# Performance work log

Hardware: AMD Instinct MI355X
Metric: run time of the kernel (lower is better)

The kernel has to match this reference:

```python
import jax, jax.numpy as jnp
import numpy as np

B, T, C = 2, 2048, 1024
N_HEAD = 16
G_NON = 32   # qgroup_size_non (layernorm / residual path)
G_LIN = 32   # qgroup_size_lin (linear path)
QMAX = 127.0
EPS = 1e-5


def quantize(x, G):
    """Group-wise symmetric int8 quantization along the last dim.
    Returns q (int8, same shape as x) and scales s with shape x.shape[:-1] + (D//G,)."""
    shp = x.shape
    xg = x.reshape(shp[:-1] + (shp[-1] // G, G))
    s = jnp.maximum(jnp.max(jnp.abs(xg), axis=-1) / QMAX, 1e-8)
    q = jnp.clip(jnp.round(xg / s[..., None]), -QMAX, QMAX).astype(jnp.int8)
    return q.reshape(shp), s


def dequant(q, s, G):
    shp = q.shape
    xg = q.astype(jnp.float32).reshape(shp[:-1] + (shp[-1] // G, G)) * s[..., None]
    return xg.reshape(shp)


def quant_dequant(x, G):
    """Fake-quantize (straight-through): forward = dequant(quantize(x))."""
    q, s = quantize(x, G)
    xd = dequant(q, s, G)
    return x + jax.lax.stop_gradient(xd - x)


def setup_inputs() -> dict:
    key = jax.random.key(0)
    k1, k2, k3, k4 = jax.random.split(key, 4)
    x = jax.random.normal(k1, (B, T, C), dtype=jnp.float32)
    # LN stats of x, produced by the previous block's int8_add_..._MeanVar
    mean = jnp.mean(x, axis=-1)
    rstd = 1.0 / jnp.sqrt(jnp.var(x, axis=-1) + EPS)
    qx, sx = quantize(x, G_NON)
    ln_w = 1.0 + 0.02 * jax.random.normal(k2, (C,), dtype=jnp.float32)
    w1 = 0.02 * jax.random.normal(k3, (3 * C, C), dtype=jnp.float32)   # c_attn.weight [out,in]
    w2 = 0.02 * jax.random.normal(k4, (C, C), dtype=jnp.float32)       # c_proj.weight [out,in]
    return {"x": x, "qx": qx.astype(jnp.int32), "sx": sx, "mean": mean,
            "rstd": rstd, "ln_w": ln_w, "w1": w1, "w2": w2}


def reference(x, qx, sx, mean, rstd, ln_w, w1, w2):
    hd = C // N_HEAD
    # ---- Part1: int8 layernorm (uses provided mean/rstd) + int8 c_attn linear ----
    ln_in = dequant(qx.astype(jnp.int8), sx, G_NON)               # [B,T,C]
    h = (ln_in - mean[..., None]) * rstd[..., None] * ln_w        # layernorm output
    hq = quant_dequant(h, G_NON)                                  # requantize activations
    w1q = quant_dequant(w1, G_LIN)                                # int8 weight
    qkv = jnp.einsum('btc,oc->bto', hq, w1q)                      # [B,T,3C]
    q, k, v = jnp.split(qkv, 3, axis=-1)
    q = q.reshape(B, T, N_HEAD, hd).transpose(0, 2, 1, 3)         # [B,H,T,hd]
    k = k.reshape(B, T, N_HEAD, hd).transpose(0, 2, 1, 3)
    v = v.reshape(B, T, N_HEAD, hd).transpose(0, 2, 1, 3)
    # ---- causal SDPA ----
    scores = jnp.einsum('bhqd,bhkd->bhqk', q, k) / jnp.sqrt(jnp.float32(hd))
    causal = jnp.tril(jnp.ones((T, T), dtype=bool))
    scores = jnp.where(causal, scores, jnp.float32(-1e30))
    attn = jax.nn.softmax(scores, axis=-1)
    y = jnp.einsum('bhqk,bhkd->bhqd', attn, v)
    y = y.transpose(0, 2, 1, 3).reshape(B, T, C)
    # ---- Part2: int8 c_proj linear + residual add with mean/var ----
    yq = quant_dequant(y, G_LIN)
    w2q = quant_dequant(w2, G_LIN)
    proj = jnp.einsum('btc,oc->bto', yq, w2q)
    fpx = x + proj                                                # fp residual output
    mean_o = jnp.mean(fpx, axis=-1)
    rstd_o = 1.0 / jnp.sqrt(jnp.var(fpx, axis=-1) + EPS)
    qo, so = quantize(fpx, G_NON)                                 # quantized output for next block
    return (fpx, qo, so, mean_o, rstd_o)
```

## Files before the change

### kernel.cpp

```cpp
#include <hip/hip_runtime.h>
#include <stdint.h>

#define BB 2
#define TT 2048
#define CC 1024
#define NH 16
#define HD 64
#define NG 32
#define ROWS (BB*TT)
#define C3 (3*CC)

typedef _Float16 half_t;
typedef __attribute__((ext_vector_type(8))) _Float16 half8;
typedef __attribute__((ext_vector_type(2))) __fp16 fp16x2;
typedef __attribute__((ext_vector_type(4))) float f32x4;

#define GLDS16(g, l) __builtin_amdgcn_global_load_lds( \
    (__attribute__((address_space(1))) void*)(g), \
    (__attribute__((address_space(3))) void*)(l), 16, 0, 0)

#define LOG2E 1.44269504f
#define DEFER_THR 5.5451774f

__device__ __forceinline__ uint32_t pk_h2(float a, float b) {
  union { fp16x2 h; uint32_t u; } cv;
  cv.h = __builtin_amdgcn_cvt_pkrtz(a, b);
  return cv.u;
}

__global__ void k_qdq_w(const float* __restrict__ w1, const float* __restrict__ w2,
                        half_t* __restrict__ o1, half_t* __restrict__ o2) {
  int g = blockIdx.x * blockDim.x + threadIdx.x;
  const float* src; half_t* dst; int gl;
  if (g < C3 * NG) { src = w1; dst = o1; gl = g; }
  else             { src = w2; dst = o2; gl = g - C3 * NG; }
  const float4* p = reinterpret_cast<const float4*>(src + (size_t)gl * 32);
  float v[32]; float amax = 0.f;
  #pragma unroll
  for (int i = 0; i < 8; ++i) {
    float4 t = p[i];
    v[4*i] = t.x; v[4*i+1] = t.y; v[4*i+2] = t.z; v[4*i+3] = t.w;
    amax = fmaxf(amax, fmaxf(fmaxf(fabsf(t.x), fabsf(t.y)), fmaxf(fabsf(t.z), fabsf(t.w))));
  }
  float s = fmaxf(amax / 127.0f, 1e-8f);
  half_t* o = dst + (size_t)gl * 32;
  #pragma unroll
  for (int c = 0; c < 4; ++c) {
    half8 ov;
    #pragma unroll
    for (int jj = 0; jj < 8; ++jj) {
      float q = fminf(fmaxf(rintf(v[c*8+jj] / s), -127.f), 127.f);
      ov[jj] = (half_t)(q * s);
    }
    *reinterpret_cast<half8*>(o + c*8) = ov;
  }
}

__global__ void k_qh(const int* __restrict__ qx, const float* __restrict__ sx,
                     const float* __restrict__ mean, const float* __restrict__ rstd,
                     const float* __restrict__ lnw, half_t* __restrict__ h16) {
  int g = blockIdx.x * blockDim.x + threadIdx.x;
  if (g >= ROWS * NG) return;
  int row = g >> 5, grp = g & 31;
  float sxv = sx[g];
  float mu = mean[row], rs = rstd[row];
  const int4* qp = reinterpret_cast<const int4*>(qx + (size_t)row * CC + grp * 32);
  const float4* wp = reinterpret_cast<const float4*>(lnw + grp * 32);
  float v[32]; float amax = 0.f;
  #pragma unroll
  for (int i = 0; i < 8; ++i) {
    int4 qv = qp[i]; float4 wv = wp[i];
    float h0 = ((float)qv.x * sxv - mu) * rs * wv.x;
    float h1 = ((float)qv.y * sxv - mu) * rs * wv.y;
    float h2 = ((float)qv.z * sxv - mu) * rs * wv.z;
    float h3 = ((float)qv.w * sxv - mu) * rs * wv.w;
    v[4*i] = h0; v[4*i+1] = h1; v[4*i+2] = h2; v[4*i+3] = h3;
    amax = fmaxf(amax, fmaxf(fmaxf(fabsf(h0), fabsf(h1)), fmaxf(fabsf(h2), fabsf(h3))));
  }
  float s = fmaxf(amax / 127.0f, 1e-8f);
  half_t* o = h16 + (size_t)row * CC + grp * 32;
  #pragma unroll
  for (int c = 0; c < 4; ++c) {
    half8 ov;
    #pragma unroll
    for (int jj = 0; jj < 8; ++jj) {
      float q = fminf(fmaxf(rintf(v[c*8+jj] / s), -127.f), 127.f);
      ov[jj] = (half_t)(q * s);
    }
    *reinterpret_cast<half8*>(o + c*8) = ov;
  }
}

template<typename TO>
__global__ __launch_bounds__(256) void k_gemm16(const half_t* __restrict__ A,
                                                const half_t* __restrict__ B,
                                                TO* __restrict__ Out, int N,
                                                int gx, int cpx, int klen) {
  __shared__ __align__(16) half_t As[128*32];
  __shared__ __align__(16) half_t Bs[128*32];
  const int tid = threadIdx.x;
  const int wave = tid >> 6, lane = tid & 63;
  const int l15 = lane & 15, lg = lane >> 4;
  const int flat = blockIdx.y * gx + blockIdx.x;
  const int swz = (flat & 7) * cpx + (flat >> 3);
  const int m0 = (swz / gx) * 128, n0 = (swz % gx) * 128;
  const int kbeg = blockIdx.z * klen;
  TO* out = Out + (size_t)blockIdx.z * ROWS * N;
  const int wm = (wave >> 1) * 64, wn = (wave & 1) * 64;
  f32x4 acc[4][4];
  #pragma unroll
  for (int i = 0; i < 4; ++i)
    #pragma unroll
    for (int jj = 0; jj < 4; ++jj) acc[i][jj] = f32x4{0.f, 0.f, 0.f, 0.f};
  const int srow = lane >> 2;
  const int scol = (lane & 3) * 8;
  const int seg0 = wave * 2;
  for (int k0 = kbeg; k0 < kbeg + klen; k0 += 32) {
    #pragma unroll
    for (int s = 0; s < 2; ++s) {
      const int seg = seg0 + s;
      GLDS16(A + (size_t)(m0 + seg*16 + srow) * 1024 + k0 + scol, As + seg*512);
      GLDS16(B + (size_t)(n0 + seg*16 + srow) * 1024 + k0 + scol, Bs + seg*512);
    }
    __syncthreads();
    half8 af[4], bf[4];
    #pragma unroll
    for (int i = 0; i < 4; ++i) {
      af[i] = *reinterpret_cast<const half8*>(As + (wm + i*16 + l15)*32 + lg*8);
      bf[i] = *reinterpret_cast<const half8*>(Bs + (wn + i*16 + l15)*32 + lg*8);
    }
    #pragma unroll
    for (int mi = 0; mi < 4; ++mi)
      #pragma unroll
      for (int ni = 0; ni < 4; ++ni)
        acc[mi][ni] = __builtin_amdgcn_mfma_f32_16x16x32_f16(af[mi], bf[ni], acc[mi][ni], 0, 0, 0);
    __syncthreads();
  }
  const int crow = m0 + wm + lg * 4;
  const int ccol = n0 + wn + l15;
  #pragma unroll
  for (int mi = 0; mi < 4; ++mi)
    #pragma unroll
    for (int ni = 0; ni < 4; ++ni)
      #pragma unroll
      for (int r = 0; r < 4; ++r)
        out[(size_t)(crow + mi*16 + r) * N + ccol + ni*16] = (TO)acc[mi][ni][r];
}

__global__ __launch_bounds__(512, 4) void k_attn16(const half_t* __restrict__ qkv,
                                                   half_t* __restrict__ y16) {
  __shared__ __align__(16) half_t Ks[2][64*72];
  __shared__ __align__(16) half_t Vt[2][64*72];
  __shared__ __align__(16) half_t Ps[8][16*72];
  const int tid = threadIdx.x;
  const int wave = tid >> 6, lane = tid & 63;
  const int l15 = lane & 15, lg = lane >> 4;
  const int w4 = wave & 3;
  const int bh = blockIdx.x, b = bh >> 4, h = bh & 15;
  const int j = blockIdx.y;
  const int qtB = 31 - j;
  const int qt = (wave >> 2) ? qtB : j;

  const size_t row = (size_t)(b * TT + qt * 64 + w4 * 16 + l15);
  const half_t* qp = qkv + row * C3 + h * HD + lg * 8;
  const half8 q0 = *reinterpret_cast<const half8*>(qp)      * (half_t)0.125f;
  const half8 q1 = *reinterpret_cast<const half8*>(qp + 32) * (half_t)0.125f;

  float m = -3.0e38f;
  f32x4 yacc[4];
  f32x4 lacc = f32x4{0,0,0,0};
  #pragma unroll
  for (int n = 0; n < 4; ++n) yacc[n] = f32x4{0,0,0,0};

  const int sj = tid >> 3, sc = (tid & 7) * 8;
  const int vkp = tid >> 4, vd0 = (tid & 15) * 4;
  const int vxor = ((vd0 >> 3) & 7) << 2;
  const int pxor = (l15 & 3) << 3;
  half_t* pw = &Ps[wave][0];

  int vdw0[4], vdw1[4];
  #pragma unroll
  for (int n = 0; n < 4; ++n) {
    const int d = n*16 + l15;
    const int x = ((n*2 + (l15 >> 3)) & 7) << 2;
    vdw0[n] = (d*36 + lg*4) ^ x;
    vdw1[n] = (d*36 + 16 + lg*4) ^ x;
  }

  half8 ones8;
  #pragma unroll
  for (int i = 0; i < 8; ++i) ones8[i] = (half_t)1.0f;

  half8 k0r; uint2 u0r, u1r;
  const half_t* kvb = qkv + ((size_t)b * TT) * C3 + CC + h * HD;
  auto kload = [&](int kt) {
    const half_t* kp = kvb + (size_t)(kt*64 + sj) * C3 + sc;
    k0r = *reinterpret_cast<const half8*>(kp);
    const half_t* vp = kvb + (size_t)(kt*64 + vkp*2) * C3 + CC + vd0;
    u0r = *reinterpret_cast<const uint2*>(vp);
    u1r = *reinterpret_cast<const uint2*>(vp + C3);
  };
  auto stage = [&](int buf) {
    *reinterpret_cast<half8*>(&Ks[buf][0] + sj*72 + sc) = k0r;
    uint32_t* vt32 = reinterpret_cast<uint32_t*>(&Vt[buf][0]);
    vt32[((vd0+0)*36 + vkp) ^ vxor] = __builtin_amdgcn_perm(u1r.x, u0r.x, 0x05040100u);
    vt32[((vd0+1)*36 + vkp) ^ vxor] = __builtin_amdgcn_perm(u1r.x, u0r.x, 0x07060302u);
    vt32[((vd0+2)*36 + vkp) ^ vxor] = __builtin_amdgcn_perm(u1r.y, u0r.y, 0x05040100u);
    vt32[((vd0+3)*36 + vkp) ^ vxor] = __builtin_amdgcn_perm(u1r.y, u0r.y, 0x07060302u);
  };

  kload(0);
  stage(0);
  kload(1);
  __syncthreads();
  for (int kt = 0; kt <= qtB; ++kt) {
    const int cur = kt & 1;
    if (kt < qtB) {
      stage(cur ^ 1);
      if (kt + 2 <= qtB) kload(kt + 2);
    }
    if (kt <= qt) {
      const half_t* ksb = &Ks[cur][0];
      const uint32_t* vt32 = reinterpret_cast<const uint32_t*>(&Vt[cur][0]);
      f32x4 sacc[4];
      __builtin_amdgcn_s_setprio(1);
      #pragma unroll
      for (int kg = 0; kg < 4; ++kg) {
        const half8 a0 = *reinterpret_cast<const half8*>(ksb + (kg*16 + l15)*72 + lg*8);
        const half8 a1 = *reinterpret_cast<const half8*>(ksb + (kg*16 + l15)*72 + lg*8 + 32);
        f32x4 t = f32x4{0,0,0,0};
        t = __builtin_amdgcn_mfma_f32_16x16x32_f16(a0, q0, t, 0, 0, 0);
        t = __builtin_amdgcn_mfma_f32_16x16x32_f16(a1, q1, t, 0, 0, 0);
        sacc[kg] = t;
      }
      __builtin_amdgcn_s_setprio(0);
      float sv[16]; float tm = -3.0e38f;
      const bool diag = (kt == qt);
      #pragma unroll
      for (int kg = 0; kg < 4; ++kg)
        #pragma unroll
        for (int r = 0; r < 4; ++r) {
          float s = sacc[kg][r];
          if (diag && (kg*16 + lg*4 + r > w4*16 + l15)) s = -1e30f;
          sv[kg*4 + r] = s;
          tm = fmaxf(tm, s);
        }
      tm = fmaxf(tm, __shfl_xor(tm, 16));
      tm = fmaxf(tm, __shfl_xor(tm, 32));
      if (!__all(tm <= m + DEFER_THR)) {
        const float mn = fmaxf(m, tm);
        const float alpha = __builtin_amdgcn_exp2f((m - mn) * LOG2E);
        #pragma unroll
        for (int n = 0; n < 4; ++n) yacc[n] *= alpha;
        lacc *= alpha;
        m = mn;
      }
      const float nm = -m * LOG2E;
      #pragma unroll
      for (int i = 0; i < 16; ++i)
        sv[i] = __builtin_amdgcn_exp2f(fmaf(sv[i], LOG2E, nm));
      uint32_t* prow = reinterpret_cast<uint32_t*>(pw) + l15*36;
      #pragma unroll
      for (int kg = 0; kg < 4; ++kg) {
        uint2 pr;
        pr.x = pk_h2(sv[kg*4 + 0], sv[kg*4 + 1]);
        pr.y = pk_h2(sv[kg*4 + 2], sv[kg*4 + 3]);
        *reinterpret_cast<uint2*>(prow + ((kg*8 + lg*2) ^ pxor)) = pr;
      }
      __builtin_amdgcn_sched_barrier(0);
      const half8 pb0 = *reinterpret_cast<const half8*>(
          pw + (l15*36 + ((lg*4) ^ pxor)) * 2);
      const half8 pb1 = *reinterpret_cast<const half8*>(
          pw + (l15*36 + ((16 + lg*4) ^ pxor)) * 2);
      __builtin_amdgcn_s_setprio(1);
      #pragma unroll
      for (int n = 0; n < 4; ++n) {
        const half8 va0 = *reinterpret_cast<const half8*>(vt32 + vdw0[n]);
        const half8 va1 = *reinterpret_cast<const half8*>(vt32 + vdw1[n]);
        yacc[n] = __builtin_amdgcn_mfma_f32_16x16x32_f16(va0, pb0, yacc[n], 0, 0, 0);
        yacc[n] = __builtin_amdgcn_mfma_f32_16x16x32_f16(va1, pb1, yacc[n], 0, 0, 0);
      }
      lacc = __builtin_amdgcn_mfma_f32_16x16x32_f16(ones8, pb0, lacc, 0, 0, 0);
      lacc = __builtin_amdgcn_mfma_f32_16x16x32_f16(ones8, pb1, lacc, 0, 0, 0);
      __builtin_amdgcn_s_setprio(0);
    }
    __syncthreads();
  }

  const float inv = 1.0f / lacc[0];
  float v[16];
  #pragma unroll
  for (int n = 0; n < 4; ++n)
    #pragma unroll
    for (int r = 0; r < 4; ++r) v[n*4 + r] = yacc[n][r] * inv;
  half_t* yp = y16 + row * CC + h * HD;
  #pragma unroll
  for (int g = 0; g < 2; ++g) {
    float am = 0.f;
    #pragma unroll
    for (int t = 0; t < 8; ++t) am = fmaxf(am, fabsf(v[g*8 + t]));
    am = fmaxf(am, __shfl_xor(am, 16));
    am = fmaxf(am, __shfl_xor(am, 32));
    const float s = fmaxf(am / 127.0f, 1e-8f);
    const float qi = 1.0f / s;
    #pragma unroll
    for (int nn = 0; nn < 2; ++nn) {
      const int n = g*2 + nn;
      union { half_t h4[4]; uint64_t u; } pk;
      #pragma unroll
      for (int r = 0; r < 4; ++r) {
        float q = fminf(fmaxf(rintf(v[n*4 + r] * qi), -127.f), 127.f);
        pk.h4[r] = (half_t)(q * s);
      }
      *reinterpret_cast<uint64_t*>(yp + n*16 + lg*4) = pk.u;
    }
  }
}

__global__ __launch_bounds__(256) void k_final(
    const float* __restrict__ x, const half_t* __restrict__ p0,
    const half_t* __restrict__ p1,
    float* __restrict__ out_fpx, float* __restrict__ out_qo, float* __restrict__ out_so,
    float* __restrict__ out_mean, float* __restrict__ out_rstd) {
  __shared__ float red[16];
  int row = blockIdx.x;
  int tid = threadIdx.x;
  size_t base = (size_t)row * CC + tid * 4;
  float4 xv = *reinterpret_cast<const float4*>(x + base);
  union { uint64_t u; half_t h[4]; } pa, pb;
  pa.u = *reinterpret_cast<const uint64_t*>(p0 + base);
  pb.u = *reinterpret_cast<const uint64_t*>(p1 + base);
  float4 f;
  f.x = xv.x + (float)pa.h[0] + (float)pb.h[0];
  f.y = xv.y + (float)pa.h[1] + (float)pb.h[1];
  f.z = xv.z + (float)pa.h[2] + (float)pb.h[2];
  f.w = xv.w + (float)pa.h[3] + (float)pb.h[3];
  *reinterpret_cast<float4*>(out_fpx + base) = f;
  float sum = f.x + f.y + f.z + f.w;
  float sq  = f.x*f.x + f.y*f.y + f.z*f.z + f.w*f.w;
  #pragma unroll
  for (int off = 1; off < 64; off <<= 1) {
    sum += __shfl_xor(sum, off);
    sq  += __shfl_xor(sq, off);
  }
  int wid = tid >> 6, lane = tid & 63;
  if (lane == 0) { red[wid] = sum; red[8 + wid] = sq; }
  __syncthreads();
  if (tid == 0) {
    float s4 = red[0] + red[1] + red[2] + red[3];
    float q4 = red[8] + red[9] + red[10] + red[11];
    float mu = s4 * (1.0f / CC);
    float var = q4 * (1.0f / CC) - mu * mu;
    out_mean[row] = mu;
    out_rstd[row] = 1.0f / sqrtf(var + 1e-5f);
  }
  float amax = fmaxf(fmaxf(fabsf(f.x), fabsf(f.y)), fmaxf(fabsf(f.z), fabsf(f.w)));
  #pragma unroll
  for (int off = 1; off < 8; off <<= 1) amax = fmaxf(amax, __shfl_xor(amax, off, 8));
  float s = fmaxf(amax / 127.0f, 1e-8f);
  int g = tid >> 3, li = tid & 7;
  if (li == 0) out_so[row * NG + g] = s;
  float4 qo;
  qo.x = fminf(fmaxf(rintf(f.x / s), -127.f), 127.f);
  qo.y = fminf(fmaxf(rintf(f.y / s), -127.f), 127.f);
  qo.z = fminf(fmaxf(rintf(f.z / s), -127.f), 127.f);
  qo.w = fminf(fmaxf(rintf(f.w / s), -127.f), 127.f);
  *reinterpret_cast<float4*>(out_qo + base) = qo;
}

extern "C" void kernel_launch(void* const* d_in, const int* in_sizes, int n_in,
                              void* d_out, int out_size, void* d_ws, size_t ws_size,
                              hipStream_t stream) {
  const float* x    = (const float*)d_in[0];
  const int*   qx   = (const int*)d_in[1];
  const float* sx   = (const float*)d_in[2];
  const float* mean = (const float*)d_in[3];
  const float* rstd = (const float*)d_in[4];
  const float* lnw  = (const float*)d_in[5];
  const float* w1   = (const float*)d_in[6];
  const float* w2   = (const float*)d_in[7];

  float* out = (float*)d_out;
  float* o_fpx  = out;
  float* o_qo   = o_fpx + (size_t)ROWS * CC;
  float* o_so   = o_qo  + (size_t)ROWS * CC;
  float* o_mean = o_so  + (size_t)ROWS * NG;
  float* o_rstd = o_mean + ROWS;

  size_t off = 0;
  char* wsb = (char*)d_ws;
  auto alloc = [&](size_t bytes) -> void* {
    void* p = wsb + off;
    off += (bytes + 255) & ~(size_t)255;
    return p;
  };
  half_t* h16   = (half_t*)alloc((size_t)ROWS * CC * 2);
  half_t* w116  = (half_t*)alloc((size_t)C3 * CC * 2);
  half_t* w216  = (half_t*)alloc((size_t)CC * CC * 2);
  half_t* qkv16 = (half_t*)alloc((size_t)ROWS * C3 * 2);
  half_t* y16   = (half_t*)alloc((size_t)ROWS * CC * 2);
  half_t* proj  = (half_t*)alloc((size_t)2 * ROWS * CC * 2);

  k_qdq_w<<<(C3 * NG + CC * NG) / 256, 256, 0, stream>>>(w1, w2, w116, w216);
  k_qh<<<(ROWS * NG) / 256, 256, 0, stream>>>(qx, sx, mean, rstd, lnw, h16);
  k_gemm16<half_t><<<dim3(C3 / 128, ROWS / 128, 1), 256, 0, stream>>>(
      h16, w116, qkv16, C3, C3 / 128, (C3 / 128) * (ROWS / 128) / 8, 1024);
  k_attn16<<<dim3(BB * NH, 16), 512, 0, stream>>>(qkv16, y16);
  k_gemm16<half_t><<<dim3(CC / 128, ROWS / 128, 2), 256, 0, stream>>>(
      y16, w216, proj, CC, CC / 128, (CC / 128) * (ROWS / 128) / 8, 512);
  k_final<<<ROWS, 256, 0, stream>>>(x, proj, proj + (size_t)ROWS * CC,
                                    o_fpx, o_qo, o_so, o_mean, o_rstd);
}
```

Measured before the change: 132.5 us.

## Process four query tiles per attention block with two 16-row sets per wave

The causal attention kernel now gives each block four query tiles (two balanced pairs) instead of two. Each wave handles 32 query rows as two 16-row sub-blocks that share every K and V fragment loaded from LDS. The grid is halved. Each K/V tile staged in shared memory is reused by more queries and there are fewer LDS reads per MFMA, at the cost of roughly doubled accumulator registers (occupancy hint lowered from 4 to 2), a larger P buffer, and fewer blocks to spread across CUs.

After: 141.0 us. +6.4%, slower.

```diff
diff --git a/kernel.cpp b/kernel.cpp
--- a/kernel.cpp
+++ b/kernel.cpp
@@ -147,36 +147,42 @@
         out[(size_t)(crow + mi*16 + r) * N + ccol + ni*16] = (TO)acc[mi][ni][r];
 }
 
-__global__ __launch_bounds__(512, 4) void k_attn16(const half_t* __restrict__ qkv,
+__global__ __launch_bounds__(512, 2) void k_attn16(const half_t* __restrict__ qkv,
                                                    half_t* __restrict__ y16) {
   __shared__ __align__(16) half_t Ks[2][64*72];
   __shared__ __align__(16) half_t Vt[2][64*72];
-  __shared__ __align__(16) half_t Ps[8][16*72];
+  __shared__ __align__(16) half_t Ps[16][16*72];
   const int tid = threadIdx.x;
   const int wave = tid >> 6, lane = tid & 63;
   const int l15 = lane & 15, lg = lane >> 4;
-  const int w4 = wave & 3;
   const int bh = blockIdx.x, b = bh >> 4, h = bh & 15;
   const int j = blockIdx.y;
-  const int qtB = 31 - j;
-  const int qt = (wave >> 2) ? qtB : j;
-
-  const size_t row = (size_t)(b * TT + qt * 64 + w4 * 16 + l15);
-  const half_t* qp = qkv + row * C3 + h * HD + lg * 8;
-  const half8 q0 = *reinterpret_cast<const half8*>(qp)      * (half_t)0.125f;
-  const half8 q1 = *reinterpret_cast<const half8*>(qp + 32) * (half_t)0.125f;
-
-  float m = -3.0e38f;
-  f32x4 yacc[4];
-  f32x4 lacc = f32x4{0,0,0,0};
-  #pragma unroll
-  for (int n = 0; n < 4; ++n) yacc[n] = f32x4{0,0,0,0};
+  const int tsel = wave >> 1;
+  const int qt = (tsel & 2) ? (30 - 2*j + (tsel & 1)) : (2*j + (tsel & 1));
+  const int rbase = (wave & 1) * 32;
+  const int ktmax = 31 - 2*j;
+
+  const size_t rowA = (size_t)(b * TT + qt * 64 + rbase + l15);
+  const size_t rowB = rowA + 16;
+  const half_t* qpA = qkv + rowA * C3 + h * HD + lg * 8;
+  const half_t* qpB = qkv + rowB * C3 + h * HD + lg * 8;
+  const half8 qA0 = *reinterpret_cast<const half8*>(qpA)      * (half_t)0.125f;
+  const half8 qA1 = *reinterpret_cast<const half8*>(qpA + 32) * (half_t)0.125f;
+  const half8 qB0 = *reinterpret_cast<const half8*>(qpB)      * (half_t)0.125f;
+  const half8 qB1 = *reinterpret_cast<const half8*>(qpB + 32) * (half_t)0.125f;
+
+  float mA = -3.0e38f, mB = -3.0e38f;
+  f32x4 yA[4], yB[4];
+  f32x4 lA = f32x4{0,0,0,0}, lB = f32x4{0,0,0,0};
+  #pragma unroll
+  for (int n = 0; n < 4; ++n) { yA[n] = f32x4{0,0,0,0}; yB[n] = f32x4{0,0,0,0}; }
 
   const int sj = tid >> 3, sc = (tid & 7) * 8;
   const int vkp = tid >> 4, vd0 = (tid & 15) * 4;
   const int vxor = ((vd0 >> 3) & 7) << 2;
   const int pxor = (l15 & 3) << 3;
-  half_t* pw = &Ps[wave][0];
+  half_t* pwA = &Ps[wave*2][0];
+  half_t* pwB = &Ps[wave*2 + 1][0];
 
   int vdw0[4], vdw1[4];
   #pragma unroll
@@ -209,112 +215,129 @@
     vt32[((vd0+3)*36 + vkp) ^ vxor] = __builtin_amdgcn_perm(u1r.y, u0r.y, 0x07060302u);
   };
 
+  auto softmax = [&](f32x4* sacc, bool diag, int rq, half_t* pw,
+                     float& m, f32x4& lacc, f32x4* yacc, half8& pb0, half8& pb1) {
+    float sv[16]; float tm = -3.0e38f;
+    #pragma unroll
+    for (int kg = 0; kg < 4; ++kg)
+      #pragma unroll
+      for (int r = 0; r < 4; ++r) {
+        float s = sacc[kg][r];
+        if (diag && (kg*16 + lg*4 + r > rq)) s = -1e30f;
+        sv[kg*4 + r] = s;
+        tm = fmaxf(tm, s);
+      }
+    tm = fmaxf(tm, __shfl_xor(tm, 16));
+    tm = fmaxf(tm, __shfl_xor(tm, 32));
+    if (!__all(tm <= m + DEFER_THR)) {
+      const float mn = fmaxf(m, tm);
+      const float alpha = __builtin_amdgcn_exp2f((m - mn) * LOG2E);
+      #pragma unroll
+      for (int n = 0; n < 4; ++n) yacc[n] *= alpha;
+      lacc *= alpha;
+      m = mn;
+    }
+    const float nm = -m * LOG2E;
+    #pragma unroll
+    for (int i = 0; i < 16; ++i)
+      sv[i] = __builtin_amdgcn_exp2f(fmaf(sv[i], LOG2E, nm));
+    uint32_t* prow = reinterpret_cast<uint32_t*>(pw) + l15*36;
+    #pragma unroll
+    for (int kg = 0; kg < 4; ++kg) {
+      uint2 pr;
+      pr.x = pk_h2(sv[kg*4 + 0], sv[kg*4 + 1]);
+      pr.y = pk_h2(sv[kg*4 + 2], sv[kg*4 + 3]);
+      *reinterpret_cast<uint2*>(prow + ((kg*8 + lg*2) ^ pxor)) = pr;
+    }
+    __builtin_amdgcn_sched_barrier(0);
+    pb0 = *reinterpret_cast<const half8*>(pw + (l15*36 + ((lg*4) ^ pxor)) * 2);
+    pb1 = *reinterpret_cast<const half8*>(pw + (l15*36 + ((16 + lg*4) ^ pxor)) * 2);
+  };
+
   kload(0);
   stage(0);
   kload(1);
   __syncthreads();
-  for (int kt = 0; kt <= qtB; ++kt) {
+  for (int kt = 0; kt <= ktmax; ++kt) {
     const int cur = kt & 1;
-    if (kt < qtB) {
+    if (kt < ktmax) {
       stage(cur ^ 1);
-      if (kt + 2 <= qtB) kload(kt + 2);
+      if (kt + 2 <= ktmax) kload(kt + 2);
     }
     if (kt <= qt) {
       const half_t* ksb = &Ks[cur][0];
       const uint32_t* vt32 = reinterpret_cast<const uint32_t*>(&Vt[cur][0]);
-      f32x4 sacc[4];
+      f32x4 sA[4], sB[4];
       __builtin_amdgcn_s_setprio(1);
       #pragma unroll
       for (int kg = 0; kg < 4; ++kg) {
         const half8 a0 = *reinterpret_cast<const half8*>(ksb + (kg*16 + l15)*72 + lg*8);
         const half8 a1 = *reinterpret_cast<const half8*>(ksb + (kg*16 + l15)*72 + lg*8 + 32);
-        f32x4 t = f32x4{0,0,0,0};
-        t = __builtin_amdgcn_mfma_f32_16x16x32_f16(a0, q0, t, 0, 0, 0);
-        t = __builtin_amdgcn_mfma_f32_16x16x32_f16(a1, q1, t, 0, 0, 0);
-        sacc[kg] = t;
+        f32x4 tA = f32x4{0,0,0,0};
+        tA = __builtin_amdgcn_mfma_f32_16x16x32_f16(a0, qA0, tA, 0, 0, 0);
+        tA = __builtin_amdgcn_mfma_f32_16x16x32_f16(a1, qA1, tA, 0, 0, 0);
+        sA[kg] = tA;
+        f32x4 tB = f32x4{0,0,0,0};
+        tB = __builtin_amdgcn_mfma_f32_16x16x32_f16(a0, qB0, tB, 0, 0, 0);
+        tB = __builtin_amdgcn_mfma_f32_16x16x32_f16(a1, qB1, tB, 0, 0, 0);
+        sB[kg] = tB;
       }
       __builtin_amdgcn_s_setprio(0);
-      float sv[16]; float tm = -3.0e38f;
       const bool diag = (kt == qt);
-      #pragma unroll
-      for (int kg = 0; kg < 4; ++kg)
-        #pragma unroll
-        for (int r = 0; r < 4; ++r) {
-          float s = sacc[kg][r];
-          if (diag && (kg*16 + lg*4 + r > w4*16 + l15)) s = -1e30f;
-          sv[kg*4 + r] = s;
-          tm = fmaxf(tm, s);
-        }
-      tm = fmaxf(tm, __shfl_xor(tm, 16));
-      tm = fmaxf(tm, __shfl_xor(tm, 32));
-      if (!__all(tm <= m + DEFER_THR)) {
-        const float mn = fmaxf(m, tm);
-        const float alpha = __builtin_amdgcn_exp2f((m - mn) * LOG2E);
-        #pragma unroll
-        for (int n = 0; n < 4; ++n) yacc[n] *= alpha;
-        lacc *= alpha;
-        m = mn;
-      }
-      const float nm = -m * LOG2E;
-      #pragma unroll
-      for (int i = 0; i < 16; ++i)
-        sv[i] = __builtin_amdgcn_exp2f(fmaf(sv[i], LOG2E, nm));
-      uint32_t* prow = reinterpret_cast<uint32_t*>(pw) + l15*36;
-      #pragma unroll
-      for (int kg = 0; kg < 4; ++kg) {
-        uint2 pr;
-        pr.x = pk_h2(sv[kg*4 + 0], sv[kg*4 + 1]);
-        pr.y = pk_h2(sv[kg*4 + 2], sv[kg*4 + 3]);
-        *reinterpret_cast<uint2*>(prow + ((kg*8 + lg*2) ^ pxor)) = pr;
-      }
-      __builtin_amdgcn_sched_barrier(0);
-      const half8 pb0 = *reinterpret_cast<const half8*>(
-          pw + (l15*36 + ((lg*4) ^ pxor)) * 2);
-      const half8 pb1 = *reinterpret_cast<const half8*>(
-          pw + (l15*36 + ((16 + lg*4) ^ pxor)) * 2);
+      half8 pA0, pA1, pB0, pB1;
+      softmax(sA, diag, rbase + l15,      pwA, mA, lA, yA, pA0, pA1);
+      softmax(sB, diag, rbase + 16 + l15, pwB, mB, lB, yB, pB0, pB1);
       __builtin_amdgcn_s_setprio(1);
       #pragma unroll
       for (int n = 0; n < 4; ++n) {
         const half8 va0 = *reinterpret_cast<const half8*>(vt32 + vdw0[n]);
         const half8 va1 = *reinterpret_cast<const half8*>(vt32 + vdw1[n]);
-        yacc[n] = __builtin_amdgcn_mfma_f32_16x16x32_f16(va0, pb0, yacc[n], 0, 0, 0);
-        yacc[n] = __builtin_amdgcn_mfma_f32_16x16x32_f16(va1, pb1, yacc[n], 0, 0, 0);
+        yA[n] = __builtin_amdgcn_mfma_f32_16x16x32_f16(va0, pA0, yA[n], 0, 0, 0);
+        yA[n] = __builtin_amdgcn_mfma_f32_16x16x32_f16(va1, pA1, yA[n], 0, 0, 0);
+        yB[n] = __builtin_amdgcn_mfma_f32_16x16x32_f16(va0, pB0, yB[n], 0, 0, 0);
+        yB[n] = __builtin_amdgcn_mfma_f32_16x16x32_f16(va1, pB1, yB[n], 0, 0, 0);
       }
-      lacc = __builtin_amdgcn_mfma_f32_16x16x32_f16(ones8, pb0, lacc, 0, 0, 0);
-      lacc = __builtin_amdgcn_mfma_f32_16x16x32_f16(ones8, pb1, lacc, 0, 0, 0);
+      lA = __builtin_amdgcn_mfma_f32_16x16x32_f16(ones8, pA0, lA, 0, 0, 0);
+      lA = __builtin_amdgcn_mfma_f32_16x16x32_f16(ones8, pA1, lA, 0, 0, 0);
+      lB = __builtin_amdgcn_mfma_f32_16x16x32_f16(ones8, pB0, lB, 0, 0, 0);
+      lB = __builtin_amdgcn_mfma_f32_16x16x32_f16(ones8, pB1, lB, 0, 0, 0);
       __builtin_amdgcn_s_setprio(0);
     }
     __syncthreads();
   }
 
-  const float inv = 1.0f / lacc[0];
-  float v[16];
-  #pragma unroll
-  for (int n = 0; n < 4; ++n)
-    #pragma unroll
-    for (int r = 0; r < 4; ++r) v[n*4 + r] = yacc[n][r] * inv;
-  half_t* yp = y16 + row * CC + h * HD;
-  #pragma unroll
-  for (int g = 0; g < 2; ++g) {
-    float am = 0.f;
-    #pragma unroll
-    for (int t = 0; t < 8; ++t) am = fmaxf(am, fabsf(v[g*8 + t]));
-    am = fmaxf(am, __shfl_xor(am, 16));
-    am = fmaxf(am, __shfl_xor(am, 32));
-    const float s = fmaxf(am / 127.0f, 1e-8f);
-    const float qi = 1.0f / s;
-    #pragma unroll
-    for (int nn = 0; nn < 2; ++nn) {
-      const int n = g*2 + nn;
-      union { half_t h4[4]; uint64_t u; } pk;
-      #pragma unroll
-      for (int r = 0; r < 4; ++r) {
-        float q = fminf(fmaxf(rintf(v[n*4 + r] * qi), -127.f), 127.f);
-        pk.h4[r] = (half_t)(q * s);
+  auto epi = [&](size_t row, float l, f32x4* yacc) {
+    const float inv = 1.0f / l;
+    float v[16];
+    #pragma unroll
+    for (int n = 0; n < 4; ++n)
+      #pragma unroll
+      for (int r = 0; r < 4; ++r) v[n*4 + r] = yacc[n][r] * inv;
+    half_t* yp = y16 + row * CC + h * HD;
+    #pragma unroll
+    for (int g = 0; g < 2; ++g) {
+      float am = 0.f;
+      #pragma unroll
+      for (int t = 0; t < 8; ++t) am = fmaxf(am, fabsf(v[g*8 + t]));
+      am = fmaxf(am, __shfl_xor(am, 16));
+      am = fmaxf(am, __shfl_xor(am, 32));
+      const float s = fmaxf(am / 127.0f, 1e-8f);
+      const float qi = 1.0f / s;
+      #pragma unroll
+      for (int nn = 0; nn < 2; ++nn) {
+        const int n = g*2 + nn;
+        union { half_t h4[4]; uint64_t u; } pk;
+        #pragma unroll
+        for (int r = 0; r < 4; ++r) {
+          float q = fminf(fmaxf(rintf(v[n*4 + r] * qi), -127.f), 127.f);
+          pk.h4[r] = (half_t)(q * s);
+        }
+        *reinterpret_cast<uint64_t*>(yp + n*16 + lg*4) = pk.u;
       }
-      *reinterpret_cast<uint64_t*>(yp + n*16 + lg*4) = pk.u;
-    }
-  }
+    }
+  };
+  epi(rowA, lA[0], yA);
+  epi(rowB, lB[0], yB);
 }
 
 __global__ __launch_bounds__(256) void k_final(
@@ -405,7 +428,7 @@
   k_qh<<<(ROWS * NG) / 256, 256, 0, stream>>>(qx, sx, mean, rstd, lnw, h16);
   k_gemm16<half_t><<<dim3(C3 / 128, ROWS / 128, 1), 256, 0, stream>>>(
       h16, w116, qkv16, C3, C3 / 128, (C3 / 128) * (ROWS / 128) / 8, 1024);
-  k_attn16<<<dim3(BB * NH, 16), 512, 0, stream>>>(qkv16, y16);
+  k_attn16<<<dim3(BB * NH, 8), 512, 0, stream>>>(qkv16, y16);
   k_gemm16<half_t><<<dim3(CC / 128, ROWS / 128, 2), 256, 0, stream>>>(
       y16, w216, proj, CC, CC / 128, (CC / 128) * (ROWS / 128) / 8, 512);
   k_final<<<ROWS, 256, 0, stream>>>(x, proj, proj + (size_t)ROWS * CC,
```
